# Performance work log

Hardware: AMD Instinct MI355X
Metric: run time of the kernel (lower is better)

Reference implementation:

```python
import jax, jax.numpy as jnp
import numpy as np

# ViT-Base/16 config
B, C, IMG, PS = 32, 3, 224, 16
D, NH, HS, HID, L, NC = 768, 12, 64, 3072, 12, 1
NP = (IMG // PS) ** 2            # 196 patches
P = NP + 1                       # +CLS = 197 tokens
EPS = 1e-5
SQRT_2_OVER_PI = 0.7978845608028654


def new_gelu(x):
    # BERT/GPT tanh-approx GELU, matching NewGELUActivation
    return 0.5 * x * (1.0 + jnp.tanh(SQRT_2_OVER_PI * (x + 0.044715 * x ** 3)))


def layernorm(x, w, b):
    m = x.mean(-1, keepdims=True)
    v = x.var(-1, keepdims=True)
    return (x - m) / jnp.sqrt(v + EPS) * w + b


def setup_inputs() -> dict:
    key = jax.random.key(0)
    ks = jax.random.split(key, 12)
    p = lambda k, shape: jax.random.normal(k, shape, jnp.float32) * 0.02
    return {
        "x": jax.random.normal(ks[0], (B, C, IMG, IMG), jnp.float32),
        "conv_w": p(ks[1], (D, C, PS, PS)),
        "conv_b": jnp.zeros((D,), jnp.float32),
        "cls_token": p(ks[2], (1, 1, D)),
        "pos_emb": p(ks[3], (1, P, D)),
        "ln1_w": jnp.ones((L, D), jnp.float32),
        "ln1_b": jnp.zeros((L, D), jnp.float32),
        "wq": p(ks[4], (L, D, D)), "bq": jnp.zeros((L, D), jnp.float32),
        "wk": p(ks[5], (L, D, D)), "bk": jnp.zeros((L, D), jnp.float32),
        "wv": p(ks[6], (L, D, D)), "bv": jnp.zeros((L, D), jnp.float32),
        "wo": p(ks[7], (L, D, D)), "bo": jnp.zeros((L, D), jnp.float32),
        "ln2_w": jnp.ones((L, D), jnp.float32),
        "ln2_b": jnp.zeros((L, D), jnp.float32),
        "w1": p(ks[8], (L, D, HID)), "b1": jnp.zeros((L, HID), jnp.float32),
        "w2": p(ks[9], (L, HID, D)), "b2": jnp.zeros((L, D), jnp.float32),
        "cls_w": p(ks[10], (D, NC)),
        "cls_b": jnp.zeros((NC,), jnp.float32),
    }


def reference(x, conv_w, conv_b, cls_token, pos_emb,
              ln1_w, ln1_b, wq, bq, wk, bk, wv, bv, wo, bo,
              ln2_w, ln2_b, w1, b1, w2, b2, cls_w, cls_b):
    Bn = x.shape[0]
    g = IMG // PS
    # conv2d with kernel=stride=patch is a patchify + matmul
    patches = x.reshape(Bn, C, g, PS, g, PS).transpose(0, 2, 4, 1, 3, 5)
    patches = patches.reshape(Bn, NP, C * PS * PS)
    h = patches @ conv_w.reshape(D, C * PS * PS).T + conv_b            # [B, NP, D]
    h = jnp.concatenate([jnp.broadcast_to(cls_token, (Bn, 1, D)), h], axis=1)
    h = h + pos_emb                                                     # [B, P, D]

    scale = 1.0 / np.sqrt(HS).astype(np.float32)

    def block(xc, pl):
        l1w, l1b, Wq, Bq, Wk, Bk, Wv, Bv, Wo, Bo, l2w, l2b, W1, B1, W2, B2 = pl
        hn = layernorm(xc, l1w, l1b)
        q = (hn @ Wq + Bq).reshape(Bn, P, NH, HS)
        k = (hn @ Wk + Bk).reshape(Bn, P, NH, HS)
        v = (hn @ Wv + Bv).reshape(Bn, P, NH, HS)
        att = jax.nn.softmax(jnp.einsum('bqhd,bkhd->bhqk', q, k) * scale, axis=-1)
        o = jnp.einsum('bhqk,bkhd->bqhd', att, v).reshape(Bn, P, D)
        xc = xc + o @ Wo + Bo
        hn2 = layernorm(xc, l2w, l2b)
        xc = xc + new_gelu(hn2 @ W1 + B1) @ W2 + B2
        return xc, None

    params = (ln1_w, ln1_b, wq, bq, wk, bk, wv, bv, wo, bo,
              ln2_w, ln2_b, w1, b1, w2, b2)
    h, _ = jax.lax.scan(block, h, params)
    return h[:, 0, :] @ cls_w + cls_b                                   # [B, NC]
```

## Files before the change

### kernel.cpp

```cpp
#include <hip/hip_runtime.h>

#define AS1 __attribute__((address_space(1)))
#define AS3 __attribute__((address_space(3)))

using f32x4  = __attribute__((ext_vector_type(4))) float;
using bf16x8 = __attribute__((ext_vector_type(8))) __bf16;

#define LAYERS 12
#define DIM    768
#define HIDDEN 3072
#define NHEAD  12
#define HSZ    64
#define BATCH  32
#define NPATCH 196
#define SEQ    197
#define MREAL  (BATCH*SEQ)
#define MPAD   6400
#define MPATCH (BATCH*NPATCH)
#define QKVN   (3*DIM)
#define KN     (DIM*DIM)

static __device__ __forceinline__ unsigned short f2b(float f){
  unsigned int u = __float_as_uint(f);
  u = (u + 0x7FFFu + ((u >> 16) & 1u)) >> 16;
  return (unsigned short)u;
}

static __device__ __forceinline__ bf16x8 u4_to_b8(uint4 u){
  union { uint4 a; bf16x8 b; } x; x.a = u; return x.b;
}

static __device__ __forceinline__ void gl_lds16(const unsigned short* g, unsigned short* l){
  __builtin_amdgcn_global_load_lds((AS1 void*)g, (AS3 void*)l, 16, 0, 0);
}

__global__ void transpose_cast(const float* __restrict__ src, unsigned short* __restrict__ dst,
                               int K, int N, size_t sls, size_t dls){
  __shared__ float tile[32][33];
  const int l  = blockIdx.z;
  const int k0 = blockIdx.x * 32;
  const int n0 = blockIdx.y * 32;
  const float* s = src + (size_t)l * sls;
  unsigned short* d = dst + (size_t)l * dls;
  const int tx = threadIdx.x & 31, ty = threadIdx.x >> 5;
#pragma unroll
  for (int r = 0; r < 32; r += 8)
    tile[ty + r][tx] = s[(size_t)(k0 + ty + r) * N + n0 + tx];
  __syncthreads();
#pragma unroll
  for (int r = 0; r < 32; r += 8)
    d[(size_t)(n0 + ty + r) * K + k0 + tx] = f2b(tile[tx][ty + r]);
}

__global__ void cast_bf16(const float* __restrict__ s, unsigned short* __restrict__ d, int n){
  int i = blockIdx.x * 256 + threadIdx.x;
  if (i < n) d[i] = f2b(s[i]);
}

__global__ void pack_bias(const float* __restrict__ bq, const float* __restrict__ bk,
                          const float* __restrict__ bv, float* __restrict__ dst){
  int i = blockIdx.x * 256 + threadIdx.x;
  if (i >= LAYERS * QKVN) return;
  int l = i / QKVN, c = i % QKVN;
  float v = (c < DIM) ? bq[l*DIM + c] : (c < 2*DIM) ? bk[l*DIM + c - DIM] : bv[l*DIM + c - 2*DIM];
  dst[i] = v;
}

__global__ void patchify(const float* __restrict__ x, unsigned short* __restrict__ pat){
  const int row = blockIdx.x;
  const int cc  = blockIdx.y * 256 + threadIdx.x;
  const int b = row / NPATCH, p = row % NPATCH;
  const int c = cc >> 8, rem = cc & 255, ii = rem >> 4, jj = rem & 15;
  const int pr = p / 14, pc = p % 14;
  float v = x[(((size_t)(b*3 + c) * 224) + pr*16 + ii) * 224 + pc*16 + jj];
  pat[(size_t)row * DIM + cc] = f2b(v);
}

__global__ void assemble(const float* __restrict__ yq, const float* __restrict__ cls,
                         const float* __restrict__ pos, float* __restrict__ h){
  const int row = blockIdx.x;
  const int d   = blockIdx.y * 256 + threadIdx.x;
  const int b = row / SEQ, p = row % SEQ;
  float v = (p == 0) ? cls[d] : yq[(size_t)(b*NPATCH + p - 1) * DIM + d];
  h[(size_t)row * DIM + d] = v + pos[p*DIM + d];
}

__global__ __launch_bounds__(256) void ln_bf16(const float* __restrict__ h,
                const float* __restrict__ w, const float* __restrict__ b,
                unsigned short* __restrict__ out, int nrows){
  const int wave = threadIdx.x >> 6, lane = threadIdx.x & 63;
  const int row = blockIdx.x * 4 + wave;
  if (row >= nrows) return;
  const float* p = h + (size_t)row * DIM;
  float4 v[3]; float s = 0.f, ss = 0.f;
#pragma unroll
  for (int t = 0; t < 3; t++){
    v[t] = *(const float4*)&p[lane*4 + t*256];
    s  += v[t].x + v[t].y + v[t].z + v[t].w;
    ss += v[t].x*v[t].x + v[t].y*v[t].y + v[t].z*v[t].z + v[t].w*v[t].w;
  }
#pragma unroll
  for (int off = 32; off; off >>= 1){ s += __shfl_xor(s, off); ss += __shfl_xor(ss, off); }
  const float mean = s * (1.f/DIM);
  const float inv  = rsqrtf(ss * (1.f/DIM) - mean*mean + 1e-5f);
#pragma unroll
  for (int t = 0; t < 3; t++){
    const int c = lane*4 + t*256;
    float4 wv = *(const float4*)&w[c];
    float4 bv = *(const float4*)&b[c];
    ushort4 o;
    o.x = f2b((v[t].x - mean)*inv*wv.x + bv.x);
    o.y = f2b((v[t].y - mean)*inv*wv.y + bv.y);
    o.z = f2b((v[t].z - mean)*inv*wv.z + bv.z);
    o.w = f2b((v[t].w - mean)*inv*wv.w + bv.w);
    *(ushort4*)&out[(size_t)row * DIM + c] = o;
  }
}

enum { EPI_F32 = 0, EPI_GELU = 1, EPI_RES = 2 };

template<int EPI>
__global__ __launch_bounds__(256) void gemm_bt(
    const unsigned short* __restrict__ A,
    const unsigned short* __restrict__ Bt,
    const float* __restrict__ bias,
    const float* __restrict__ resid,
    float* __restrict__ Cf,
    unsigned short* __restrict__ Cb,
    int K, int N)
{
  __shared__ unsigned short As[4096];
  __shared__ unsigned short Bs[4096];
  const int tid = threadIdx.x;
  const int m0 = blockIdx.x * 128, n0 = blockIdx.y * 128;
  const int lane = tid & 63, wave = tid >> 6;
  const int wr = wave >> 1, wc = wave & 1;
  const int lr = lane & 15, lg = lane >> 4;

  const unsigned short* ga = A  + (size_t)(m0 + (tid >> 2)) * K + (tid & 3) * 8;
  const unsigned short* gb = Bt + (size_t)(n0 + (tid >> 2)) * K + (tid & 3) * 8;
  const size_t rstep = (size_t)64 * K;
  unsigned short* lA = &As[tid * 8];
  unsigned short* lB = &Bs[tid * 8];

  f32x4 acc[4][4];
#pragma unroll
  for (int i = 0; i < 4; i++)
#pragma unroll
    for (int j = 0; j < 4; j++) acc[i][j] = f32x4{0.f, 0.f, 0.f, 0.f};

  for (int kt = 0; kt < K; kt += 32){
    gl_lds16(ga + kt,         lA);
    gl_lds16(ga + kt + rstep, lA + 2048);
    gl_lds16(gb + kt,         lB);
    gl_lds16(gb + kt + rstep, lB + 2048);
    __syncthreads();
    bf16x8 af[4], bg[4];
#pragma unroll
    for (int i = 0; i < 4; i++) af[i] = *(const bf16x8*)&As[(wr*64 + i*16 + lr)*32 + lg*8];
#pragma unroll
    for (int j = 0; j < 4; j++) bg[j] = *(const bf16x8*)&Bs[(wc*64 + j*16 + lr)*32 + lg*8];
#pragma unroll
    for (int i = 0; i < 4; i++)
#pragma unroll
      for (int j = 0; j < 4; j++)
        acc[i][j] = __builtin_amdgcn_mfma_f32_16x16x32_bf16(af[i], bg[j], acc[i][j], 0, 0, 0);
    __syncthreads();
  }

#pragma unroll
  for (int i = 0; i < 4; i++){
    const int row = m0 + wr*64 + i*16 + lg*4;
#pragma unroll
    for (int q = 0; q < 4; q++){
      const size_t rbase = (size_t)(row + q) * N;
#pragma unroll
      for (int j = 0; j < 4; j++){
        const int col = n0 + wc*64 + j*16 + lr;
        float v = acc[i][j][q] + bias[col];
        if constexpr (EPI == EPI_F32){
          Cf[rbase + col] = v;
        } else if constexpr (EPI == EPI_RES){
          Cf[rbase + col] = v + resid[rbase + col];
        } else {
          float u = 0.7978845608028654f * (v + 0.044715f * v*v*v);
          float g = v / (1.f + __expf(-2.f * u));
          Cb[rbase + col] = f2b(g);
        }
      }
    }
  }
}

__global__ __launch_bounds__(512) void attn_mfma(const float* __restrict__ qkv,
                                                 unsigned short* __restrict__ ob){
  __shared__ unsigned short Ks[208*64];
  __shared__ unsigned short Vt[64*256];
  __shared__ unsigned short Ps[8*14*256];
  const int hh = blockIdx.x, b = blockIdx.y;
  const int tid = threadIdx.x, w = tid >> 6, lane = tid & 63;
  const int c = lane & 15, g = lane >> 4;
  const float* base = qkv + (size_t)b * SEQ * QKVN;
  char* KsB = (char*)Ks;
  char* VtB = (char*)Vt;
  char* PsB = (char*)(Ps + w * 3584);

  for (int i = tid; i < 3584; i += 512) ((uint4*)Ps)[i] = make_uint4(0,0,0,0);

  for (int cc = tid; cc < 208*8; cc += 512){
    const int r = cc >> 3, d0 = (cc & 7) * 8;
    uint4 u = make_uint4(0,0,0,0);
    if (r < SEQ){
      const float* p = base + (size_t)r*QKVN + DIM + hh*HSZ + d0;
      float4 f0 = *(const float4*)p;
      float4 f1 = *(const float4*)(p + 4);
      u.x = f2b(f0.x) | ((unsigned)f2b(f0.y) << 16);
      u.y = f2b(f0.z) | ((unsigned)f2b(f0.w) << 16);
      u.z = f2b(f1.x) | ((unsigned)f2b(f1.y) << 16);
      u.w = f2b(f1.z) | ((unsigned)f2b(f1.w) << 16);
    }
    *(uint4*)(KsB + r*128 + ((d0*2) ^ ((r & 7) << 4))) = u;
  }
  for (int cc = tid; cc < 224*16; cc += 512){
    const int k = cc >> 4, d0 = (cc & 15) * 4;
    float4 f = make_float4(0.f, 0.f, 0.f, 0.f);
    if (k < SEQ) f = *(const float4*)(base + (size_t)k*QKVN + 2*DIM + hh*HSZ + d0);
    unsigned short h0 = f2b(f.x), h1 = f2b(f.y), h2 = f2b(f.z), h3 = f2b(f.w);
    *(unsigned short*)(VtB + (d0+0)*512 + ((2*k) ^ (((d0+0) & 7) << 4))) = h0;
    *(unsigned short*)(VtB + (d0+1)*512 + ((2*k) ^ (((d0+1) & 7) << 4))) = h1;
    *(unsigned short*)(VtB + (d0+2)*512 + ((2*k) ^ (((d0+2) & 7) << 4))) = h2;
    *(unsigned short*)(VtB + (d0+3)*512 + ((2*k) ^ (((d0+3) & 7) << 4))) = h3;
  }
  __syncthreads();

  const float scale = 0.125f;
  for (int qt = w; qt < 13; qt += 8){
    bf16x8 qf[2];
    {
      const float* qp = base + (size_t)(qt*16 + c)*QKVN + hh*HSZ + g*8;
#pragma unroll
      for (int s = 0; s < 2; s++){
        float4 f0 = *(const float4*)(qp + 32*s);
        float4 f1 = *(const float4*)(qp + 32*s + 4);
        uint4 u;
        u.x = f2b(f0.x*scale) | ((unsigned)f2b(f0.y*scale) << 16);
        u.y = f2b(f0.z*scale) | ((unsigned)f2b(f0.w*scale) << 16);
        u.z = f2b(f1.x*scale) | ((unsigned)f2b(f1.y*scale) << 16);
        u.w = f2b(f1.z*scale) | ((unsigned)f2b(f1.w*scale) << 16);
        qf[s] = u4_to_b8(u);
      }
    }
    f32x4 acc[13];
#pragma unroll
    for (int j = 0; j < 13; j++) acc[j] = f32x4{0.f, 0.f, 0.f, 0.f};
#pragma unroll
    for (int j = 0; j < 13; j++){
#pragma unroll
      for (int s = 0; s < 2; s++){
        const int kr = j*16 + c;
        bf16x8 kf = *(const bf16x8*)(KsB + kr*128 + ((16*g + 64*s) ^ ((kr & 7) << 4)));
        acc[j] = __builtin_amdgcn_mfma_f32_16x16x32_bf16(qf[s], kf, acc[j], 0, 0, 0);
      }
    }
    if (c >= 5){ acc[12][0] = -1e30f; acc[12][1] = -1e30f; acc[12][2] = -1e30f; acc[12][3] = -1e30f; }
    float inv[4];
#pragma unroll
    for (int r = 0; r < 4; r++){
      float m = acc[0][r];
#pragma unroll
      for (int j = 1; j < 13; j++) m = fmaxf(m, acc[j][r]);
      m = fmaxf(m, __shfl_xor(m, 1)); m = fmaxf(m, __shfl_xor(m, 2));
      m = fmaxf(m, __shfl_xor(m, 4)); m = fmaxf(m, __shfl_xor(m, 8));
      float s = 0.f;
#pragma unroll
      for (int j = 0; j < 13; j++){ float e = __expf(acc[j][r] - m); acc[j][r] = e; s += e; }
      s += __shfl_xor(s, 1); s += __shfl_xor(s, 2); s += __shfl_xor(s, 4); s += __shfl_xor(s, 8);
      inv[r] = 1.f / s;
    }
#pragma unroll
    for (int j = 0; j < 13; j++){
#pragma unroll
      for (int r = 0; r < 4; r++){
        if (j < 12 || c < 5){
          const int row = g*4 + r;
          *(unsigned short*)(PsB + j*512 + (row & 3)*128 + (row >> 2)*32 + 2*c) = f2b(acc[j][r]);
        }
      }
    }
    asm volatile("s_waitcnt lgkmcnt(0)" ::: "memory");
    __builtin_amdgcn_sched_barrier(0);
    f32x4 oacc[4];
#pragma unroll
    for (int dt = 0; dt < 4; dt++) oacc[dt] = f32x4{0.f, 0.f, 0.f, 0.f};
#pragma unroll
    for (int ks = 0; ks < 7; ks++){
      const int j = 2*ks + (g >> 1);
      bf16x8 pf = *(const bf16x8*)(PsB + j*512 + (c & 3)*128 + (c >> 2)*32 + 16*(g & 1));
#pragma unroll
      for (int dt = 0; dt < 4; dt++){
        const int d = dt*16 + c;
        bf16x8 vf = *(const bf16x8*)(VtB + d*512 + ((16*g + 64*ks) ^ ((d & 7) << 4)));
        oacc[dt] = __builtin_amdgcn_mfma_f32_16x16x32_bf16(pf, vf, oacc[dt], 0, 0, 0);
      }
    }
#pragma unroll
    for (int dt = 0; dt < 4; dt++){
#pragma unroll
      for (int r = 0; r < 4; r++){
        const int rt = qt*16 + g*4 + r;
        if (rt < SEQ)
          ob[(size_t)(b*SEQ + rt)*DIM + hh*HSZ + dt*16 + c] = f2b(oacc[dt][r] * inv[r]);
      }
    }
  }
}

__global__ void classifier(const float* __restrict__ h, const float* __restrict__ cw,
                           const float* __restrict__ cb, float* __restrict__ out){
  const int b = blockIdx.x, tid = threadIdx.x, lane = tid & 63, wave = tid >> 6;
  const float* p = h + (size_t)b * SEQ * DIM;
  float s = 0.f;
  for (int c = tid; c < DIM; c += 256) s += p[c] * cw[c];
#pragma unroll
  for (int off = 32; off; off >>= 1) s += __shfl_xor(s, off);
  __shared__ float red[4];
  if (lane == 0) red[wave] = s;
  __syncthreads();
  if (tid == 0) out[b] = red[0] + red[1] + red[2] + red[3] + cb[0];
}

extern "C" void kernel_launch(void* const* d_in, const int* in_sizes, int n_in,
                              void* d_out, int out_size, void* d_ws, size_t ws_size,
                              hipStream_t stream)
{
  (void)in_sizes; (void)n_in; (void)out_size; (void)ws_size;
  const float* x      = (const float*)d_in[0];
  const float* conv_w = (const float*)d_in[1];
  const float* conv_b = (const float*)d_in[2];
  const float* cls_tk = (const float*)d_in[3];
  const float* pos    = (const float*)d_in[4];
  const float* ln1w   = (const float*)d_in[5];
  const float* ln1b   = (const float*)d_in[6];
  const float* wq     = (const float*)d_in[7];
  const float* bq     = (const float*)d_in[8];
  const float* wk     = (const float*)d_in[9];
  const float* bk     = (const float*)d_in[10];
  const float* wv     = (const float*)d_in[11];
  const float* bv     = (const float*)d_in[12];
  const float* wo     = (const float*)d_in[13];
  const float* bo     = (const float*)d_in[14];
  const float* ln2w   = (const float*)d_in[15];
  const float* ln2b   = (const float*)d_in[16];
  const float* w1     = (const float*)d_in[17];
  const float* b1     = (const float*)d_in[18];
  const float* w2     = (const float*)d_in[19];
  const float* b2     = (const float*)d_in[20];
  const float* cls_w  = (const float*)d_in[21];
  const float* cls_b  = (const float*)d_in[22];
  float* out = (float*)d_out;

  char* wp = (char*)d_ws;
  auto take = [&](size_t bytes) -> void* {
    void* p = (void*)wp;
    wp += (bytes + 255) & ~(size_t)255;
    return p;
  };
  unsigned short* wtA = (unsigned short*)take((size_t)LAYERS*4*KN*2);
  unsigned short* wt1 = (unsigned short*)take((size_t)LAYERS*DIM*HIDDEN*2);
  unsigned short* wt2 = (unsigned short*)take((size_t)LAYERS*DIM*HIDDEN*2);
  unsigned short* cwb = (unsigned short*)take((size_t)KN*2);
  float*          bqkv= (float*)take((size_t)LAYERS*QKVN*4);
  unsigned short* pat = (unsigned short*)take((size_t)MPATCH*DIM*2);
  float*          h   = (float*)take((size_t)MPAD*DIM*4);
  unsigned short* hn  = (unsigned short*)take((size_t)MPAD*DIM*2);
  float*          qkv = (float*)take((size_t)MPAD*QKVN*4);
  unsigned short* ob  = (unsigned short*)take((size_t)MPAD*DIM*2);
  unsigned short* mid = (unsigned short*)take((size_t)MPAD*HIDDEN*2);

  transpose_cast<<<dim3(DIM/32, DIM/32, LAYERS), 256, 0, stream>>>(wq, wtA + 0*KN, DIM, DIM, (size_t)KN, (size_t)4*KN);
  transpose_cast<<<dim3(DIM/32, DIM/32, LAYERS), 256, 0, stream>>>(wk, wtA + 1*KN, DIM, DIM, (size_t)KN, (size_t)4*KN);
  transpose_cast<<<dim3(DIM/32, DIM/32, LAYERS), 256, 0, stream>>>(wv, wtA + 2*KN, DIM, DIM, (size_t)KN, (size_t)4*KN);
  transpose_cast<<<dim3(DIM/32, DIM/32, LAYERS), 256, 0, stream>>>(wo, wtA + 3*KN, DIM, DIM, (size_t)KN, (size_t)4*KN);
  transpose_cast<<<dim3(DIM/32, HIDDEN/32, LAYERS), 256, 0, stream>>>(w1, wt1, DIM, HIDDEN, (size_t)DIM*HIDDEN, (size_t)DIM*HIDDEN);
  transpose_cast<<<dim3(HIDDEN/32, DIM/32, LAYERS), 256, 0, stream>>>(w2, wt2, HIDDEN, DIM, (size_t)DIM*HIDDEN, (size_t)DIM*HIDDEN);
  cast_bf16<<<(KN + 255)/256, 256, 0, stream>>>(conv_w, cwb, KN);
  pack_bias<<<(LAYERS*QKVN + 255)/256, 256, 0, stream>>>(bq, bk, bv, bqkv);

  patchify<<<dim3(MPATCH, 3), 256, 0, stream>>>(x, pat);
  gemm_bt<EPI_F32><<<dim3(MPATCH/128, DIM/128), 256, 0, stream>>>(pat, cwb, conv_b, nullptr, qkv, nullptr, DIM, DIM);
  assemble<<<dim3(MREAL, 3), 256, 0, stream>>>(qkv, cls_tk, pos, h);

  for (int l = 0; l < LAYERS; ++l){
    ln_bf16<<<MREAL/4, 256, 0, stream>>>(h, ln1w + l*DIM, ln1b + l*DIM, hn, MREAL);
    gemm_bt<EPI_F32><<<dim3(MPAD/128, QKVN/128), 256, 0, stream>>>(
        hn, wtA + (size_t)l*4*KN, bqkv + l*QKVN, nullptr, qkv, nullptr, DIM, QKVN);
    attn_mfma<<<dim3(NHEAD, BATCH), 512, 0, stream>>>(qkv, ob);
    gemm_bt<EPI_RES><<<dim3(MPAD/128, DIM/128), 256, 0, stream>>>(
        ob, wtA + ((size_t)l*4 + 3)*KN, bo + l*DIM, h, h, nullptr, DIM, DIM);
    ln_bf16<<<MREAL/4, 256, 0, stream>>>(h, ln2w + l*DIM, ln2b + l*DIM, hn, MREAL);
    gemm_bt<EPI_GELU><<<dim3(MPAD/128, HIDDEN/128), 256, 0, stream>>>(
        hn, wt1 + (size_t)l*DIM*HIDDEN, b1 + l*HIDDEN, nullptr, nullptr, mid, DIM, HIDDEN);
    gemm_bt<EPI_RES><<<dim3(MPAD/128, DIM/128), 256, 0, stream>>>(
        mid, wt2 + (size_t)l*DIM*HIDDEN, b2 + l*DIM, h, h, nullptr, HIDDEN, DIM);
  }

  classifier<<<BATCH, 256, 0, stream>>>(h, cls_w, cls_b, out);
}
```

Measured before the change: 3.905 ms.

## Double-buffer GEMM LDS, swizzle chunks, store QKV as bf16, narrow N tiles

The GEMM now double-buffers its LDS tiles so the next K-slice loads while the current one runs on MFMA, and swizzles 16-byte chunks to reduce LDS bank conflicts. The grid is reordered so N-tiles vary fastest, and a BN=64 variant gives the N=768 GEMMs more blocks. The QKV GEMM writes bf16 instead of fp32, which halves that traffic and removes the conversions in attention. The softmax scale is now applied to the fp32 scores rather than to Q before rounding, which slightly changes numerics.

```diff
diff --git a/kernel.cpp b/kernel.cpp
--- a/kernel.cpp
+++ b/kernel.cpp
@@ -26,10 +26,6 @@
   return (unsigned short)u;
 }
 
-static __device__ __forceinline__ bf16x8 u4_to_b8(uint4 u){
-  union { uint4 a; bf16x8 b; } x; x.a = u; return x.b;
-}
-
 static __device__ __forceinline__ void gl_lds16(const unsigned short* g, unsigned short* l){
   __builtin_amdgcn_global_load_lds((AS1 void*)g, (AS3 void*)l, 16, 0, 0);
 }
@@ -117,9 +113,9 @@
   }
 }
 
-enum { EPI_F32 = 0, EPI_GELU = 1, EPI_RES = 2 };
-
-template<int EPI>
+enum { EPI_F32 = 0, EPI_GELU = 1, EPI_RES = 2, EPI_B16 = 3 };
+
+template<int EPI, int BN>
 __global__ __launch_bounds__(256) void gemm_bt(
     const unsigned short* __restrict__ A,
     const unsigned short* __restrict__ Bt,
@@ -129,44 +125,58 @@
     unsigned short* __restrict__ Cb,
     int K, int N)
 {
-  __shared__ unsigned short As[4096];
-  __shared__ unsigned short Bs[4096];
+  constexpr int NJ = BN / 32;
+  __shared__ unsigned short As[2][4096];
+  __shared__ unsigned short Bs[2][BN*32];
   const int tid = threadIdx.x;
-  const int m0 = blockIdx.x * 128, n0 = blockIdx.y * 128;
+  const int n0 = blockIdx.x * BN, m0 = blockIdx.y * 128;
   const int lane = tid & 63, wave = tid >> 6;
   const int wr = wave >> 1, wc = wave & 1;
   const int lr = lane & 15, lg = lane >> 4;
 
-  const unsigned short* ga = A  + (size_t)(m0 + (tid >> 2)) * K + (tid & 3) * 8;
-  const unsigned short* gb = Bt + (size_t)(n0 + (tid >> 2)) * K + (tid & 3) * 8;
+  const int schunk = (tid & 3) ^ ((tid >> 3) & 3);
+  const unsigned short* ga = A  + (size_t)(m0 + (tid >> 2)) * K + schunk * 8;
+  const unsigned short* gb = Bt + (size_t)(n0 + (tid >> 2)) * K + schunk * 8;
   const size_t rstep = (size_t)64 * K;
-  unsigned short* lA = &As[tid * 8];
-  unsigned short* lB = &Bs[tid * 8];
-
-  f32x4 acc[4][4];
+
+  f32x4 acc[4][NJ];
 #pragma unroll
   for (int i = 0; i < 4; i++)
 #pragma unroll
-    for (int j = 0; j < 4; j++) acc[i][j] = f32x4{0.f, 0.f, 0.f, 0.f};
-
-  for (int kt = 0; kt < K; kt += 32){
-    gl_lds16(ga + kt,         lA);
-    gl_lds16(ga + kt + rstep, lA + 2048);
-    gl_lds16(gb + kt,         lB);
-    gl_lds16(gb + kt + rstep, lB + 2048);
+    for (int j = 0; j < NJ; j++) acc[i][j] = f32x4{0.f, 0.f, 0.f, 0.f};
+
+  auto stage = [&](int bf, int kt){
+    gl_lds16(ga + kt,         &As[bf][tid*8]);
+    gl_lds16(ga + kt + rstep, &As[bf][2048 + tid*8]);
+    gl_lds16(gb + kt,         &Bs[bf][tid*8]);
+    if constexpr (BN == 128) gl_lds16(gb + kt + rstep, &Bs[bf][2048 + tid*8]);
+  };
+  const int rchunk = (lg ^ ((lr >> 1) & 3)) * 8;
+  auto compute = [&](int bf){
+    bf16x8 af[4], bg[NJ];
+#pragma unroll
+    for (int i = 0; i < 4; i++)
+      af[i] = *(const bf16x8*)&As[bf][(wr*64 + i*16 + lr)*32 + rchunk];
+#pragma unroll
+    for (int j = 0; j < NJ; j++)
+      bg[j] = *(const bf16x8*)&Bs[bf][(wc*(BN/2) + j*16 + lr)*32 + rchunk];
+#pragma unroll
+    for (int i = 0; i < 4; i++)
+#pragma unroll
+      for (int j = 0; j < NJ; j++)
+        acc[i][j] = __builtin_amdgcn_mfma_f32_16x16x32_bf16(af[i], bg[j], acc[i][j], 0, 0, 0);
+  };
+
+  stage(0, 0);
+  __syncthreads();
+  int cur = 0;
+  for (int kt = 32; kt < K; kt += 32){
+    stage(cur ^ 1, kt);
+    compute(cur);
     __syncthreads();
-    bf16x8 af[4], bg[4];
-#pragma unroll
-    for (int i = 0; i < 4; i++) af[i] = *(const bf16x8*)&As[(wr*64 + i*16 + lr)*32 + lg*8];
-#pragma unroll
-    for (int j = 0; j < 4; j++) bg[j] = *(const bf16x8*)&Bs[(wc*64 + j*16 + lr)*32 + lg*8];
-#pragma unroll
-    for (int i = 0; i < 4; i++)
-#pragma unroll
-      for (int j = 0; j < 4; j++)
-        acc[i][j] = __builtin_amdgcn_mfma_f32_16x16x32_bf16(af[i], bg[j], acc[i][j], 0, 0, 0);
-    __syncthreads();
-  }
+    cur ^= 1;
+  }
+  compute(cur);
 
 #pragma unroll
   for (int i = 0; i < 4; i++){
@@ -175,13 +185,15 @@
     for (int q = 0; q < 4; q++){
       const size_t rbase = (size_t)(row + q) * N;
 #pragma unroll
-      for (int j = 0; j < 4; j++){
-        const int col = n0 + wc*64 + j*16 + lr;
+      for (int j = 0; j < NJ; j++){
+        const int col = n0 + wc*(BN/2) + j*16 + lr;
         float v = acc[i][j][q] + bias[col];
         if constexpr (EPI == EPI_F32){
           Cf[rbase + col] = v;
         } else if constexpr (EPI == EPI_RES){
           Cf[rbase + col] = v + resid[rbase + col];
+        } else if constexpr (EPI == EPI_B16){
+          Cb[rbase + col] = f2b(v);
         } else {
           float u = 0.7978845608028654f * (v + 0.044715f * v*v*v);
           float g = v / (1.f + __expf(-2.f * u));
@@ -192,7 +204,7 @@
   }
 }
 
-__global__ __launch_bounds__(512) void attn_mfma(const float* __restrict__ qkv,
+__global__ __launch_bounds__(512) void attn_mfma(const unsigned short* __restrict__ qkvb,
                                                  unsigned short* __restrict__ ob){
   __shared__ unsigned short Ks[208*64];
   __shared__ unsigned short Vt[64*256];
@@ -200,7 +212,7 @@
   const int hh = blockIdx.x, b = blockIdx.y;
   const int tid = threadIdx.x, w = tid >> 6, lane = tid & 63;
   const int c = lane & 15, g = lane >> 4;
-  const float* base = qkv + (size_t)b * SEQ * QKVN;
+  const unsigned short* base = qkvb + (size_t)b * SEQ * QKVN;
   char* KsB = (char*)Ks;
   char* VtB = (char*)Vt;
   char* PsB = (char*)(Ps + w * 3584);
@@ -210,57 +222,39 @@
   for (int cc = tid; cc < 208*8; cc += 512){
     const int r = cc >> 3, d0 = (cc & 7) * 8;
     uint4 u = make_uint4(0,0,0,0);
-    if (r < SEQ){
-      const float* p = base + (size_t)r*QKVN + DIM + hh*HSZ + d0;
-      float4 f0 = *(const float4*)p;
-      float4 f1 = *(const float4*)(p + 4);
-      u.x = f2b(f0.x) | ((unsigned)f2b(f0.y) << 16);
-      u.y = f2b(f0.z) | ((unsigned)f2b(f0.w) << 16);
-      u.z = f2b(f1.x) | ((unsigned)f2b(f1.y) << 16);
-      u.w = f2b(f1.z) | ((unsigned)f2b(f1.w) << 16);
-    }
+    if (r < SEQ) u = *(const uint4*)(base + (size_t)r*QKVN + DIM + hh*HSZ + d0);
     *(uint4*)(KsB + r*128 + ((d0*2) ^ ((r & 7) << 4))) = u;
   }
   for (int cc = tid; cc < 224*16; cc += 512){
     const int k = cc >> 4, d0 = (cc & 15) * 4;
-    float4 f = make_float4(0.f, 0.f, 0.f, 0.f);
-    if (k < SEQ) f = *(const float4*)(base + (size_t)k*QKVN + 2*DIM + hh*HSZ + d0);
-    unsigned short h0 = f2b(f.x), h1 = f2b(f.y), h2 = f2b(f.z), h3 = f2b(f.w);
-    *(unsigned short*)(VtB + (d0+0)*512 + ((2*k) ^ (((d0+0) & 7) << 4))) = h0;
-    *(unsigned short*)(VtB + (d0+1)*512 + ((2*k) ^ (((d0+1) & 7) << 4))) = h1;
-    *(unsigned short*)(VtB + (d0+2)*512 + ((2*k) ^ (((d0+2) & 7) << 4))) = h2;
-    *(unsigned short*)(VtB + (d0+3)*512 + ((2*k) ^ (((d0+3) & 7) << 4))) = h3;
+    ushort4 f = make_ushort4(0,0,0,0);
+    if (k < SEQ) f = *(const ushort4*)(base + (size_t)k*QKVN + 2*DIM + hh*HSZ + d0);
+    *(unsigned short*)(VtB + (d0+0)*512 + ((2*k) ^ (((d0+0) & 7) << 4))) = f.x;
+    *(unsigned short*)(VtB + (d0+1)*512 + ((2*k) ^ (((d0+1) & 7) << 4))) = f.y;
+    *(unsigned short*)(VtB + (d0+2)*512 + ((2*k) ^ (((d0+2) & 7) << 4))) = f.z;
+    *(unsigned short*)(VtB + (d0+3)*512 + ((2*k) ^ (((d0+3) & 7) << 4))) = f.w;
   }
   __syncthreads();
 
   const float scale = 0.125f;
   for (int qt = w; qt < 13; qt += 8){
-    bf16x8 qf[2];
-    {
-      const float* qp = base + (size_t)(qt*16 + c)*QKVN + hh*HSZ + g*8;
-#pragma unroll
-      for (int s = 0; s < 2; s++){
-        float4 f0 = *(const float4*)(qp + 32*s);
-        float4 f1 = *(const float4*)(qp + 32*s + 4);
-        uint4 u;
-        u.x = f2b(f0.x*scale) | ((unsigned)f2b(f0.y*scale) << 16);
-        u.y = f2b(f0.z*scale) | ((unsigned)f2b(f0.w*scale) << 16);
-        u.z = f2b(f1.x*scale) | ((unsigned)f2b(f1.y*scale) << 16);
-        u.w = f2b(f1.z*scale) | ((unsigned)f2b(f1.w*scale) << 16);
-        qf[s] = u4_to_b8(u);
-      }
-    }
+    const unsigned short* qp = base + (size_t)(qt*16 + c)*QKVN + hh*HSZ + g*8;
+    bf16x8 qf0 = *(const bf16x8*)qp;
+    bf16x8 qf1 = *(const bf16x8*)(qp + 32);
     f32x4 acc[13];
 #pragma unroll
     for (int j = 0; j < 13; j++) acc[j] = f32x4{0.f, 0.f, 0.f, 0.f};
 #pragma unroll
     for (int j = 0; j < 13; j++){
-#pragma unroll
-      for (int s = 0; s < 2; s++){
-        const int kr = j*16 + c;
-        bf16x8 kf = *(const bf16x8*)(KsB + kr*128 + ((16*g + 64*s) ^ ((kr & 7) << 4)));
-        acc[j] = __builtin_amdgcn_mfma_f32_16x16x32_bf16(qf[s], kf, acc[j], 0, 0, 0);
-      }
+      const int kr = j*16 + c;
+      bf16x8 k0 = *(const bf16x8*)(KsB + kr*128 + ((16*g) ^ ((kr & 7) << 4)));
+      bf16x8 k1 = *(const bf16x8*)(KsB + kr*128 + ((16*g + 64) ^ ((kr & 7) << 4)));
+      acc[j] = __builtin_amdgcn_mfma_f32_16x16x32_bf16(qf0, k0, acc[j], 0, 0, 0);
+      acc[j] = __builtin_amdgcn_mfma_f32_16x16x32_bf16(qf1, k1, acc[j], 0, 0, 0);
+    }
+#pragma unroll
+    for (int j = 0; j < 13; j++){
+      acc[j][0] *= scale; acc[j][1] *= scale; acc[j][2] *= scale; acc[j][3] *= scale;
     }
     if (c >= 5){ acc[12][0] = -1e30f; acc[12][1] = -1e30f; acc[12][2] = -1e30f; acc[12][3] = -1e30f; }
     float inv[4];
@@ -365,17 +359,18 @@
     wp += (bytes + 255) & ~(size_t)255;
     return p;
   };
-  unsigned short* wtA = (unsigned short*)take((size_t)LAYERS*4*KN*2);
-  unsigned short* wt1 = (unsigned short*)take((size_t)LAYERS*DIM*HIDDEN*2);
-  unsigned short* wt2 = (unsigned short*)take((size_t)LAYERS*DIM*HIDDEN*2);
-  unsigned short* cwb = (unsigned short*)take((size_t)KN*2);
-  float*          bqkv= (float*)take((size_t)LAYERS*QKVN*4);
-  unsigned short* pat = (unsigned short*)take((size_t)MPATCH*DIM*2);
-  float*          h   = (float*)take((size_t)MPAD*DIM*4);
-  unsigned short* hn  = (unsigned short*)take((size_t)MPAD*DIM*2);
-  float*          qkv = (float*)take((size_t)MPAD*QKVN*4);
-  unsigned short* ob  = (unsigned short*)take((size_t)MPAD*DIM*2);
-  unsigned short* mid = (unsigned short*)take((size_t)MPAD*HIDDEN*2);
+  unsigned short* wtA  = (unsigned short*)take((size_t)LAYERS*4*KN*2);
+  unsigned short* wt1  = (unsigned short*)take((size_t)LAYERS*DIM*HIDDEN*2);
+  unsigned short* wt2  = (unsigned short*)take((size_t)LAYERS*DIM*HIDDEN*2);
+  unsigned short* cwb  = (unsigned short*)take((size_t)KN*2);
+  float*          bqkv = (float*)take((size_t)LAYERS*QKVN*4);
+  unsigned short* pat  = (unsigned short*)take((size_t)MPATCH*DIM*2);
+  float*          pemb = (float*)take((size_t)MPATCH*DIM*4);
+  float*          h    = (float*)take((size_t)MPAD*DIM*4);
+  unsigned short* hn   = (unsigned short*)take((size_t)MPAD*DIM*2);
+  unsigned short* qkvb = (unsigned short*)take((size_t)MPAD*QKVN*2);
+  unsigned short* ob   = (unsigned short*)take((size_t)MPAD*DIM*2);
+  unsigned short* mid  = (unsigned short*)take((size_t)MPAD*HIDDEN*2);
 
   transpose_cast<<<dim3(DIM/32, DIM/32, LAYERS), 256, 0, stream>>>(wq, wtA + 0*KN, DIM, DIM, (size_t)KN, (size_t)4*KN);
   transpose_cast<<<dim3(DIM/32, DIM/32, LAYERS), 256, 0, stream>>>(wk, wtA + 1*KN, DIM, DIM, (size_t)KN, (size_t)4*KN);
@@ -387,20 +382,20 @@
   pack_bias<<<(LAYERS*QKVN + 255)/256, 256, 0, stream>>>(bq, bk, bv, bqkv);
 
   patchify<<<dim3(MPATCH, 3), 256, 0, stream>>>(x, pat);
-  gemm_bt<EPI_F32><<<dim3(MPATCH/128, DIM/128), 256, 0, stream>>>(pat, cwb, conv_b, nullptr, qkv, nullptr, DIM, DIM);
-  assemble<<<dim3(MREAL, 3), 256, 0, stream>>>(qkv, cls_tk, pos, h);
+  gemm_bt<EPI_F32,64><<<dim3(DIM/64, MPATCH/128), 256, 0, stream>>>(pat, cwb, conv_b, nullptr, pemb, nullptr, DIM, DIM);
+  assemble<<<dim3(MREAL, 3), 256, 0, stream>>>(pemb, cls_tk, pos, h);
 
   for (int l = 0; l < LAYERS; ++l){
     ln_bf16<<<MREAL/4, 256, 0, stream>>>(h, ln1w + l*DIM, ln1b + l*DIM, hn, MREAL);
-    gemm_bt<EPI_F32><<<dim3(MPAD/128, QKVN/128), 256, 0, stream>>>(
-        hn, wtA + (size_t)l*4*KN, bqkv + l*QKVN, nullptr, qkv, nullptr, DIM, QKVN);
-    attn_mfma<<<dim3(NHEAD, BATCH), 512, 0, stream>>>(qkv, ob);
-    gemm_bt<EPI_RES><<<dim3(MPAD/128, DIM/128), 256, 0, stream>>>(
+    gemm_bt<EPI_B16,128><<<dim3(QKVN/128, MPAD/128), 256, 0, stream>>>(
+        hn, wtA + (size_t)l*4*KN, bqkv + l*QKVN, nullptr, nullptr, qkvb, DIM, QKVN);
+    attn_mfma<<<dim3(NHEAD, BATCH), 512, 0, stream>>>(qkvb, ob);
+    gemm_bt<EPI_RES,64><<<dim3(DIM/64, MPAD/128), 256, 0, stream>>>(
         ob, wtA + ((size_t)l*4 + 3)*KN, bo + l*DIM, h, h, nullptr, DIM, DIM);
     ln_bf16<<<MREAL/4, 256, 0, stream>>>(h, ln2w + l*DIM, ln2b + l*DIM, hn, MREAL);
-    gemm_bt<EPI_GELU><<<dim3(MPAD/128, HIDDEN/128), 256, 0, stream>>>(
+    gemm_bt<EPI_GELU,128><<<dim3(HIDDEN/128, MPAD/128), 256, 0, stream>>>(
         hn, wt1 + (size_t)l*DIM*HIDDEN, b1 + l*HIDDEN, nullptr, nullptr, mid, DIM, HIDDEN);
-    gemm_bt<EPI_RES><<<dim3(MPAD/128, DIM/128), 256, 0, stream>>>(
+    gemm_bt<EPI_RES,64><<<dim3(DIM/64, MPAD/128), 256, 0, stream>>>(
         mid, wt2 + (size_t)l*DIM*HIDDEN, b2 + l*DIM, h, h, nullptr, HIDDEN, DIM);
   }
 
```

Measured after the change: 3.290 ms. 1.19x faster.
